# Performance work log

Measured on AMD Instinct MI355X. Metric: run time of the kernel, lower is better.

Reference implementation:

```python
import jax, jax.numpy as jnp
import numpy as np

N_AQI = 35
N_MEO = 18
H = N_AQI + 3 * N_MEO  # 89
T = 120
B = 32768


def setup_inputs() -> dict:
    key = jax.random.key(0)
    ks = jax.random.split(key, 9)
    s = 1.0 / np.sqrt(H)
    return {
        "out": jax.random.normal(ks[0], (B, T, H), dtype=jnp.float32),
        # GRUCell params (PyTorch layout: [3H, in], gate order r,z,n)
        "W_ih": jax.random.normal(ks[1], (3 * H, H), dtype=jnp.float32) * s,
        "W_hh": jax.random.normal(ks[2], (3 * H, H), dtype=jnp.float32) * s,
        "b_ih": jax.random.normal(ks[3], (3 * H,), dtype=jnp.float32) * s,
        "b_hh": jax.random.normal(ks[4], (3 * H,), dtype=jnp.float32) * s,
        # metric_fc: 89 -> 32
        "W_m": jax.random.normal(ks[5], (32, H), dtype=jnp.float32) * s,
        "b_m": jax.random.normal(ks[6], (32,), dtype=jnp.float32) * s,
        # output_fc: 32 -> 1
        "W_o": jax.random.normal(ks[7], (1, 32), dtype=jnp.float32) * (1.0 / np.sqrt(32)),
        "b_o": jax.random.normal(ks[8], (1,), dtype=jnp.float32) * (1.0 / np.sqrt(32)),
    }


def reference(out, W_ih, W_hh, b_ih, b_hh, W_m, b_m, W_o, b_o):
    h0 = jnp.zeros((out.shape[0], H), dtype=out.dtype)
    xs = jnp.transpose(out[:, :T, :], (1, 0, 2))  # (T, B, H)

    def step(h, x):
        gi = x @ W_ih.T + b_ih          # (B, 3H)
        gh = h @ W_hh.T + b_hh          # (B, 3H)
        i_r, i_z, i_n = jnp.split(gi, 3, axis=-1)
        h_r, h_z, h_n = jnp.split(gh, 3, axis=-1)
        r = jax.nn.sigmoid(i_r + h_r)
        z = jax.nn.sigmoid(i_z + h_z)
        n = jnp.tanh(i_n + r * h_n)
        h_new = (1.0 - z) * n + z * h   # PyTorch GRUCell update
        return h_new, None

    h, _ = jax.lax.scan(step, h0, xs)
    out_mmetric = jax.nn.sigmoid(h @ W_m.T + b_m)        # (B, 32)
    out_mscore = jax.nn.sigmoid(out_mmetric @ W_o.T + b_o)  # (B, 1)
    return out_mscore, out_mmetric
```

## Files before the change

kernel.cpp:

```cpp
#include <hip/hip_runtime.h>
#include <hip/hip_bf16.h>

#define Hn   89
#define Tn   120
#define BM   128
#define LDP  104
#define NTHR 768

using bf16   = __bf16;
using bf16x8 = __attribute__((ext_vector_type(8))) __bf16;
typedef __attribute__((ext_vector_type(4))) float f32x4;

__device__ __forceinline__ f32x4 ld4(const float* p) {
  f32x4 v; __builtin_memcpy(&v, p, 16); return v;
}
__device__ __forceinline__ bf16x8 pack8(f32x4 a, f32x4 b) {
  bf16x8 r;
  r[0]=(bf16)a[0]; r[1]=(bf16)a[1]; r[2]=(bf16)a[2]; r[3]=(bf16)a[3];
  r[4]=(bf16)b[0]; r[5]=(bf16)b[1]; r[6]=(bf16)b[2]; r[7]=(bf16)b[3];
  return r;
}
__device__ __forceinline__ float fsig(float x) {
  return __builtin_amdgcn_rcpf(1.f + __builtin_amdgcn_exp2f(-1.44269504f * x));
}
__device__ __forceinline__ float ftanh(float x) {
  return 1.f - 2.f * __builtin_amdgcn_rcpf(1.f + __builtin_amdgcn_exp2f(2.88539008f * x));
}

__global__ __launch_bounds__(NTHR, 3)
void gru_fused(const float* __restrict__ X,
               const float* __restrict__ Wih,
               const float* __restrict__ Whh,
               const float* __restrict__ bih,
               const float* __restrict__ bhh,
               const float* __restrict__ Wm,
               const float* __restrict__ bm,
               const float* __restrict__ Wo,
               const float* __restrict__ bo,
               float* __restrict__ Y,
               int Bt)
{
  __shared__ __align__(16) bf16 Xl[2][BM][LDP];
  __shared__ __align__(16) bf16 Hl[2][BM][LDP];
  __shared__ float Ml[BM][32];

  const int tid  = threadIdx.x;
  const int lane = tid & 63;
  const int wv   = tid >> 6;
  const int jt   = wv >> 1;
  const int hf   = wv & 1;
  const int l15  = lane & 15;
  const int kg   = lane >> 4;
  const int j    = jt * 16 + l15;
  const bool jok = (j < Hn);
  const int swz  = (l15 >> 2) & 3;
  const size_t brow0 = (size_t)blockIdx.x * BM;

  bf16x8 Bf[3][2][3];
#pragma unroll
  for (int g = 0; g < 3; ++g)
#pragma unroll
    for (int s = 0; s < 2; ++s) {
      const float* W = s ? Whh : Wih;
#pragma unroll
      for (int kt = 0; kt < 3; ++kt) {
        bf16x8 f;
        const int k0 = kt * 32 + kg * 8;
#pragma unroll
        for (int e = 0; e < 8; ++e) {
          const int k = k0 + e;
          float v = 0.f;
          if (jok) {
            if (k < Hn) v = W[(size_t)(g * Hn + j) * Hn + k];
            else if (k == Hn) {
              if (g < 2) v = s ? 0.f : (bih[g * Hn + j] + bhh[g * Hn + j]);
              else       v = s ? bhh[2 * Hn + j] : bih[2 * Hn + j];
            }
          }
          f[e] = (bf16)v;
        }
        Bf[g][s][kt] = f;
      }
    }

  int soff0, soff1, loff0, loff1;
  bool lst0, lst1;
  {
    const int p0 = tid, p1 = tid + NTHR;
    const int r0 = p0 / 12, s0 = p0 - r0 * 12;
    const int r1 = p1 / 12, s1 = p1 - r1 * 12;
    lst0 = (s0 == 11); lst1 = (s1 == 11);
    soff0 = r0 * (Tn * Hn) + s0 * 8;  loff0 = r0 * LDP + s0 * 8;
    soff1 = r1 * (Tn * Hn) + s1 * 8;  loff1 = r1 * LDP + s1 * 8;
  }
  const float* Xb2 = X + brow0 * (size_t)(Tn * Hn);
  f32x4 A0, B0, A1, B1;

  auto issue = [&](int toff) {
    const float* p0 = Xb2 + soff0 + toff;
    const float* p1 = Xb2 + soff1 + toff;
    if (lst0) { f32x4 a = {p0[0], 1.0f, 0.f, 0.f}; A0 = a; B0 = (f32x4){0.f,0.f,0.f,0.f}; }
    else      { A0 = ld4(p0); B0 = ld4(p0 + 4); }
    if (lst1) { f32x4 a = {p1[0], 1.0f, 0.f, 0.f}; A1 = a; B1 = (f32x4){0.f,0.f,0.f,0.f}; }
    else      { A1 = ld4(p1); B1 = ld4(p1 + 4); }
  };
  auto commit = [&](int plane) {
    *(bf16x8*)(&Xl[plane][0][0] + loff0) = pack8(A0, B0);
    *(bf16x8*)(&Xl[plane][0][0] + loff1) = pack8(A1, B1);
  };

  if (tid < 2 * BM) {
    const int pl = tid >> 7, r = tid & (BM - 1);
    bf16* hp = &Hl[pl][r][(size_t)((11 ^ ((r >> 2) & 3)) << 3)];
    hp[1] = (bf16)1.0f;
#pragma unroll
    for (int e = 2; e < 8; ++e) hp[e] = (bf16)0.f;
  }

  float hold[4][4];
#pragma unroll
  for (int mt = 0; mt < 4; ++mt)
#pragma unroll
    for (int q = 0; q < 4; ++q) hold[mt][q] = 0.f;

  const int hswzcol = (((j >> 3) ^ kg) << 3) | (j & 7);
  bf16*       hwb = &Hl[0][0][0] + (hf * 64 + kg * 4) * LDP + hswzcol;
  const bf16* xrb = &Xl[0][0][0] + (hf * 64 + l15) * LDP + kg * 8;
  const bf16* hrb = &Hl[0][0][0] + (hf * 64 + l15) * LDP + ((kg ^ swz) << 3);
  const int bufo = BM * LDP;

  issue(0);
  if (jok) {
#pragma unroll
    for (int mt = 0; mt < 4; ++mt)
#pragma unroll
      for (int q = 0; q < 4; ++q)
        hwb[(mt * 16 + q) * LDP] = (bf16)0.f;
  }
  commit(0);

  int toff = Hn;
  for (int t = 0; t < Tn; ++t) {
    const int b = t & 1;
    __syncthreads();
    const bool pf = (t + 1 < Tn);
    if (pf) issue(toff);

    __builtin_amdgcn_s_setprio(1);
    const bf16* xr = xrb + b * bufo;
    const bf16* hr = hrb + b * bufo;
    bf16*       hw = hwb + (b ^ 1) * bufo;
#pragma unroll
    for (int mt = 0; mt < 4; ++mt) {
      f32x4 ar = {0,0,0,0}, az = {0,0,0,0}, ain = {0,0,0,0}, ahn = {0,0,0,0};
#pragma unroll
      for (int kt = 0; kt < 3; ++kt) {
        const bf16x8 ax = *(const bf16x8*)(xr + mt * 16 * LDP + kt * 32);
        const bf16x8 ah = *(const bf16x8*)(hr + mt * 16 * LDP + kt * 32);
        ar  = __builtin_amdgcn_mfma_f32_16x16x32_bf16(ax, Bf[0][0][kt], ar, 0, 0, 0);
        ar  = __builtin_amdgcn_mfma_f32_16x16x32_bf16(ah, Bf[0][1][kt], ar, 0, 0, 0);
        az  = __builtin_amdgcn_mfma_f32_16x16x32_bf16(ax, Bf[1][0][kt], az, 0, 0, 0);
        az  = __builtin_amdgcn_mfma_f32_16x16x32_bf16(ah, Bf[1][1][kt], az, 0, 0, 0);
        ain = __builtin_amdgcn_mfma_f32_16x16x32_bf16(ax, Bf[2][0][kt], ain, 0, 0, 0);
        ahn = __builtin_amdgcn_mfma_f32_16x16x32_bf16(ah, Bf[2][1][kt], ahn, 0, 0, 0);
      }
#pragma unroll
      for (int q = 0; q < 4; ++q) {
        const float r_ = fsig(ar[q]);
        const float z_ = fsig(az[q]);
        const float n_ = ftanh(ain[q] + r_ * ahn[q]);
        hold[mt][q] = n_ + z_ * (hold[mt][q] - n_);
      }
      if (jok) {
#pragma unroll
        for (int q = 0; q < 4; ++q)
          hw[(mt * 16 + q) * LDP] = (bf16)hold[mt][q];
      }
    }
    __builtin_amdgcn_s_setprio(0);
    if (pf) { commit(b ^ 1); toff += Hn; }
  }
  __syncthreads();

  for (int p = tid; p < BM * 32; p += NTHR) {
    const int r = p >> 5, c = p & 31;
    const int rs = (r >> 2) & 3;
    const bf16* hr2 = &Hl[0][r][0];
    const float* wrow = Wm + c * Hn;
    float acc = bm[c];
#pragma unroll 4
    for (int cb = 0; cb < 11; ++cb) {
      const bf16x8 hv = *(const bf16x8*)(hr2 + ((cb ^ rs) << 3));
      const f32x4 wa = ld4(wrow + cb * 8);
      const f32x4 wb = ld4(wrow + cb * 8 + 4);
      acc = fmaf((float)hv[0], wa[0], acc); acc = fmaf((float)hv[1], wa[1], acc);
      acc = fmaf((float)hv[2], wa[2], acc); acc = fmaf((float)hv[3], wa[3], acc);
      acc = fmaf((float)hv[4], wb[0], acc); acc = fmaf((float)hv[5], wb[1], acc);
      acc = fmaf((float)hv[6], wb[2], acc); acc = fmaf((float)hv[7], wb[3], acc);
    }
    acc = fmaf((float)hr2[(11 ^ rs) << 3], wrow[88], acc);
    const float mv = fsig(acc);
    Ml[r][c] = mv;
    Y[(size_t)Bt + (brow0 + r) * 32 + c] = mv;
  }
  __syncthreads();
  if (tid < BM) {
    float acc = bo[0];
#pragma unroll
    for (int c = 0; c < 32; ++c) acc = fmaf(Ml[tid][c], Wo[c], acc);
    Y[brow0 + tid] = fsig(acc);
  }
}

extern "C" void kernel_launch(void* const* d_in, const int* in_sizes, int n_in,
                              void* d_out, int out_size, void* d_ws, size_t ws_size,
                              hipStream_t stream) {
  const float* X   = (const float*)d_in[0];
  const float* Wih = (const float*)d_in[1];
  const float* Whh = (const float*)d_in[2];
  const float* bih = (const float*)d_in[3];
  const float* bhh = (const float*)d_in[4];
  const float* Wm  = (const float*)d_in[5];
  const float* bm  = (const float*)d_in[6];
  const float* Wo  = (const float*)d_in[7];
  const float* bo  = (const float*)d_in[8];

  const int B = in_sizes[0] / (Tn * Hn);
  dim3 grid(B / BM), block(NTHR);
  gru_fused<<<grid, block, 0, stream>>>(X, Wih, Whh, bih, bhh, Wm, bm, Wo, bo,
                                        (float*)d_out, B);
}
```

Before: 624.6 us.

## Transpose GRU MFMA output layout to vectorize hidden-state stores

Swaps the MFMA operands so each lane's accumulator holds four consecutive hidden units for one batch row rather than four batch rows for one unit. The new hidden state can then be written to LDS as a single bf16x4 store instead of four scalar stores, and the XOR swizzle on the H buffer is dropped. The recurrent n-gate bias is now added in fp32 instead of through a constant-one column in H. The r and z input/hidden products also get separate accumulators, which shortens the dependent MFMA chains. Risks are LDS bank conflicts without the swizzle and a few extra VALU adds per element.

```diff
diff --git a/kernel.cpp b/kernel.cpp
--- a/kernel.cpp
+++ b/kernel.cpp
@@ -8,6 +8,7 @@
 #define NTHR 768
 
 using bf16   = __bf16;
+using bf16x4 = __attribute__((ext_vector_type(4))) __bf16;
 using bf16x8 = __attribute__((ext_vector_type(8))) __bf16;
 typedef __attribute__((ext_vector_type(4))) float f32x4;
 
@@ -51,9 +52,9 @@
   const int hf   = wv & 1;
   const int l15  = lane & 15;
   const int kg   = lane >> 4;
-  const int j    = jt * 16 + l15;
-  const bool jok = (j < Hn);
-  const int swz  = (l15 >> 2) & 3;
+  const int jA   = jt * 16 + l15;
+  const bool jAok = (jA < Hn);
+  const int j0   = jt * 16 + kg * 4;
   const size_t brow0 = (size_t)blockIdx.x * BM;
 
   bf16x8 Bf[3][2][3];
@@ -70,18 +71,22 @@
         for (int e = 0; e < 8; ++e) {
           const int k = k0 + e;
           float v = 0.f;
-          if (jok) {
-            if (k < Hn) v = W[(size_t)(g * Hn + j) * Hn + k];
-            else if (k == Hn) {
-              if (g < 2) v = s ? 0.f : (bih[g * Hn + j] + bhh[g * Hn + j]);
-              else       v = s ? bhh[2 * Hn + j] : bih[2 * Hn + j];
-            }
+          if (jAok) {
+            if (k < Hn) v = W[(size_t)(g * Hn + jA) * Hn + k];
+            else if (k == Hn && s == 0)
+              v = (g < 2) ? (bih[g * Hn + jA] + bhh[g * Hn + jA])
+                          : bih[2 * Hn + jA];
           }
           f[e] = (bf16)v;
         }
         Bf[g][s][kt] = f;
       }
     }
+
+  float bhnq[4];
+#pragma unroll
+  for (int q = 0; q < 4; ++q)
+    bhnq[q] = (j0 + q < Hn) ? bhh[2 * Hn + j0 + q] : 0.f;
 
   int soff0, soff1, loff0, loff1;
   bool lst0, lst1;
@@ -109,34 +114,24 @@
     *(bf16x8*)(&Xl[plane][0][0] + loff1) = pack8(A1, B1);
   };
 
-  if (tid < 2 * BM) {
-    const int pl = tid >> 7, r = tid & (BM - 1);
-    bf16* hp = &Hl[pl][r][(size_t)((11 ^ ((r >> 2) & 3)) << 3)];
-    hp[1] = (bf16)1.0f;
-#pragma unroll
-    for (int e = 2; e < 8; ++e) hp[e] = (bf16)0.f;
-  }
-
   float hold[4][4];
 #pragma unroll
   for (int mt = 0; mt < 4; ++mt)
 #pragma unroll
     for (int q = 0; q < 4; ++q) hold[mt][q] = 0.f;
 
-  const int hswzcol = (((j >> 3) ^ kg) << 3) | (j & 7);
-  bf16*       hwb = &Hl[0][0][0] + (hf * 64 + kg * 4) * LDP + hswzcol;
+  bf16*       hwb = &Hl[0][0][0] + (hf * 64 + l15) * LDP + j0;
   const bf16* xrb = &Xl[0][0][0] + (hf * 64 + l15) * LDP + kg * 8;
-  const bf16* hrb = &Hl[0][0][0] + (hf * 64 + l15) * LDP + ((kg ^ swz) << 3);
+  const bf16* hrb = &Hl[0][0][0] + (hf * 64 + l15) * LDP + kg * 8;
   const int bufo = BM * LDP;
 
+  {
+    const bf16x4 z4 = {(bf16)0.f, (bf16)0.f, (bf16)0.f, (bf16)0.f};
+#pragma unroll
+    for (int mt = 0; mt < 4; ++mt)
+      *(bf16x4*)(hwb + mt * 16 * LDP) = z4;
+  }
   issue(0);
-  if (jok) {
-#pragma unroll
-    for (int mt = 0; mt < 4; ++mt)
-#pragma unroll
-      for (int q = 0; q < 4; ++q)
-        hwb[(mt * 16 + q) * LDP] = (bf16)0.f;
-  }
   commit(0);
 
   int toff = Hn;
@@ -152,30 +147,31 @@
     bf16*       hw = hwb + (b ^ 1) * bufo;
 #pragma unroll
     for (int mt = 0; mt < 4; ++mt) {
-      f32x4 ar = {0,0,0,0}, az = {0,0,0,0}, ain = {0,0,0,0}, ahn = {0,0,0,0};
+      f32x4 ari = {0,0,0,0}, arh = {0,0,0,0};
+      f32x4 azi = {0,0,0,0}, azh = {0,0,0,0};
+      f32x4 ain = {0,0,0,0}, ahn = {0,0,0,0};
 #pragma unroll
       for (int kt = 0; kt < 3; ++kt) {
-        const bf16x8 ax = *(const bf16x8*)(xr + mt * 16 * LDP + kt * 32);
-        const bf16x8 ah = *(const bf16x8*)(hr + mt * 16 * LDP + kt * 32);
-        ar  = __builtin_amdgcn_mfma_f32_16x16x32_bf16(ax, Bf[0][0][kt], ar, 0, 0, 0);
-        ar  = __builtin_amdgcn_mfma_f32_16x16x32_bf16(ah, Bf[0][1][kt], ar, 0, 0, 0);
-        az  = __builtin_amdgcn_mfma_f32_16x16x32_bf16(ax, Bf[1][0][kt], az, 0, 0, 0);
-        az  = __builtin_amdgcn_mfma_f32_16x16x32_bf16(ah, Bf[1][1][kt], az, 0, 0, 0);
-        ain = __builtin_amdgcn_mfma_f32_16x16x32_bf16(ax, Bf[2][0][kt], ain, 0, 0, 0);
-        ahn = __builtin_amdgcn_mfma_f32_16x16x32_bf16(ah, Bf[2][1][kt], ahn, 0, 0, 0);
+        const bf16x8 bx = *(const bf16x8*)(xr + mt * 16 * LDP + kt * 32);
+        const bf16x8 bh = *(const bf16x8*)(hr + mt * 16 * LDP + kt * 32);
+        ari = __builtin_amdgcn_mfma_f32_16x16x32_bf16(Bf[0][0][kt], bx, ari, 0, 0, 0);
+        arh = __builtin_amdgcn_mfma_f32_16x16x32_bf16(Bf[0][1][kt], bh, arh, 0, 0, 0);
+        azi = __builtin_amdgcn_mfma_f32_16x16x32_bf16(Bf[1][0][kt], bx, azi, 0, 0, 0);
+        azh = __builtin_amdgcn_mfma_f32_16x16x32_bf16(Bf[1][1][kt], bh, azh, 0, 0, 0);
+        ain = __builtin_amdgcn_mfma_f32_16x16x32_bf16(Bf[2][0][kt], bx, ain, 0, 0, 0);
+        ahn = __builtin_amdgcn_mfma_f32_16x16x32_bf16(Bf[2][1][kt], bh, ahn, 0, 0, 0);
       }
+      bf16x4 wv4;
 #pragma unroll
       for (int q = 0; q < 4; ++q) {
-        const float r_ = fsig(ar[q]);
-        const float z_ = fsig(az[q]);
-        const float n_ = ftanh(ain[q] + r_ * ahn[q]);
-        hold[mt][q] = n_ + z_ * (hold[mt][q] - n_);
+        const float r_ = fsig(ari[q] + arh[q]);
+        const float z_ = fsig(azi[q] + azh[q]);
+        const float n_ = ftanh(ain[q] + r_ * (ahn[q] + bhnq[q]));
+        const float hv = n_ + z_ * (hold[mt][q] - n_);
+        hold[mt][q] = hv;
+        wv4[q] = (bf16)hv;
       }
-      if (jok) {
-#pragma unroll
-        for (int q = 0; q < 4; ++q)
-          hw[(mt * 16 + q) * LDP] = (bf16)hold[mt][q];
-      }
+      *(bf16x4*)(hw + mt * 16 * LDP) = wv4;
     }
     __builtin_amdgcn_s_setprio(0);
     if (pf) { commit(b ^ 1); toff += Hn; }
@@ -184,13 +180,12 @@
 
   for (int p = tid; p < BM * 32; p += NTHR) {
     const int r = p >> 5, c = p & 31;
-    const int rs = (r >> 2) & 3;
     const bf16* hr2 = &Hl[0][r][0];
     const float* wrow = Wm + c * Hn;
     float acc = bm[c];
 #pragma unroll 4
     for (int cb = 0; cb < 11; ++cb) {
-      const bf16x8 hv = *(const bf16x8*)(hr2 + ((cb ^ rs) << 3));
+      const bf16x8 hv = *(const bf16x8*)(hr2 + cb * 8);
       const f32x4 wa = ld4(wrow + cb * 8);
       const f32x4 wb = ld4(wrow + cb * 8 + 4);
       acc = fmaf((float)hv[0], wa[0], acc); acc = fmaf((float)hv[1], wa[1], acc);
@@ -198,7 +193,7 @@
       acc = fmaf((float)hv[4], wb[0], acc); acc = fmaf((float)hv[5], wb[1], acc);
       acc = fmaf((float)hv[6], wb[2], acc); acc = fmaf((float)hv[7], wb[3], acc);
     }
-    acc = fmaf((float)hr2[(11 ^ rs) << 3], wrow[88], acc);
+    acc = fmaf((float)hr2[88], wrow[88], acc);
     const float mv = fsig(acc);
     Ml[r][c] = mv;
     Y[(size_t)Bt + (brow0 + r) * 32 + c] = mv;
```

Result: no change. 627.5 us (+0.5%).
